# Performance work log

Hardware: AMD Instinct MI355X
Metric: run time of the kernel (lower is better)

Reference implementation:

```python
import jax, jax.numpy as jnp
import numpy as np

IN_DIM = 768
OUT_DIM = 4096
N_SK_ITER = 3
TARGET_TEMP = 0.06
PRED_TEMP = 0.12
PREFACTOR = 1.0
EXP_MAX = 50.0  # exp_max_values[float32]
SK_EPS = 1e-8
NORM_EPS = 1e-7


def setup_inputs() -> dict:
    key = jax.random.key(0)
    kx, kw = jax.random.split(key)
    x = jax.random.normal(kx, (16, 1024, IN_DIM), dtype=jnp.float32)
    # nn.Linear weight init: normal(std=1); bias zeros
    weight = jax.random.normal(kw, (OUT_DIM, IN_DIM), dtype=jnp.float32)
    bias = jnp.zeros((OUT_DIM,), dtype=jnp.float32)
    return {"x": x, "weight": weight, "bias": bias}


def sinkhorn_knopp(M, n_iterations, eps=SK_EPS):
    # stable_exp: shift by max over dim=-2 (token axis), add EXP_MAX
    shift = jnp.max(M, axis=-2, keepdims=True)
    M = jnp.exp(M + EXP_MAX - shift)
    for _ in range(n_iterations):  # small fixed count
        M = M / (jnp.sum(M, axis=-2, keepdims=True) + eps)  # column normalize
        M = M / (jnp.sum(M, axis=-1, keepdims=True) + eps)  # row normalize
    return M


def reference(x, weight, bias):
    # L2 normalize features (eps matches torch F.normalize with p=2)
    norm = jnp.maximum(jnp.linalg.norm(x, axis=-1, keepdims=True), NORM_EPS)
    x_n = x / norm
    logits = jnp.einsum("bnd,kd->bnk", x_n, weight) + bias  # [B, N, K]
    # positionwise_sk=True: no flatten before sinkhorn; detach -> stop_gradient
    assignments = sinkhorn_knopp(jax.lax.stop_gradient(logits) / TARGET_TEMP, N_SK_ITER)
    tgt = assignments.reshape(-1, OUT_DIM).astype(jnp.float32)
    pred = logits.reshape(-1, OUT_DIM).astype(jnp.float32)
    loss = -jnp.mean(jnp.sum(tgt * jax.nn.log_softmax(pred / PRED_TEMP, axis=-1), axis=-1))
    return assignments, PREFACTOR * loss
```

## Files before the change

kernel.cpp:

```cpp
#include <hip/hip_runtime.h>
#include <math.h>

#define BATCH 16
#define NTOK  1024
#define NCLU  4096
#define DIM   768
#define MROWS (BATCH * NTOK)

constexpr float TT_INV    = 16.666666666666668f;
constexpr float PT_INV    = 8.333333333333334f;
constexpr float SK_EPS_   = 1e-8f;
constexpr float NORM_EPS_ = 1e-7f;
constexpr float COL_SHIFT = 60.0f;
constexpr float P_SHIFT   = 40.0f;

typedef _Float16 f16x8 __attribute__((ext_vector_type(8)));
typedef _Float16 f16x4 __attribute__((ext_vector_type(4)));
typedef float    f32x4 __attribute__((ext_vector_type(4)));

struct F8 { float v[8]; };

__device__ __forceinline__ F8 load8(const float* p) {
    const float4 a = *(const float4*)p;
    const float4 b = *(const float4*)(p + 4);
    return F8{{a.x, a.y, a.z, a.w, b.x, b.y, b.z, b.w}};
}
__device__ __forceinline__ F8 load8(const _Float16* p) {
    f16x8 h = *(const f16x8*)p;
    F8 r;
#pragma unroll
    for (int i = 0; i < 8; ++i) r.v[i] = (float)h[i];
    return r;
}

__device__ __forceinline__ float wave_sum(float s) {
#pragma unroll
    for (int off = 32; off; off >>= 1) s += __shfl_xor(s, off);
    return s;
}

__device__ __forceinline__ void gl_lds16(const void* g, void* l) {
    __builtin_amdgcn_global_load_lds(
        (const __attribute__((address_space(1))) unsigned int*)g,
        (__attribute__((address_space(3))) unsigned int*)l,
        16, 0, 0);
}

__global__ __launch_bounds__(256) void castx_kernel(
    const float* __restrict__ x, _Float16* __restrict__ x16)
{
    int row  = (blockIdx.x * 256 + threadIdx.x) >> 6;
    int lane = threadIdx.x & 63;
    const float4* rp = (const float4*)(x + (size_t)row * DIM);
    float4 v[3];
    float ss = 0.f;
#pragma unroll
    for (int i = 0; i < 3; ++i) {
        v[i] = rp[lane + i * 64];
        ss += v[i].x * v[i].x + v[i].y * v[i].y + v[i].z * v[i].z + v[i].w * v[i].w;
    }
    ss = wave_sum(ss);
    float sc = 1.0f / fmaxf(sqrtf(ss), NORM_EPS_);
    _Float16* op = x16 + (size_t)row * DIM;
#pragma unroll
    for (int i = 0; i < 3; ++i) {
        f16x4 h;
        h[0] = (_Float16)(v[i].x * sc); h[1] = (_Float16)(v[i].y * sc);
        h[2] = (_Float16)(v[i].z * sc); h[3] = (_Float16)(v[i].w * sc);
        *(f16x4*)(op + 4 * (lane + i * 64)) = h;
    }
}

__global__ __launch_bounds__(256) void castw_kernel(
    const float* __restrict__ w, _Float16* __restrict__ w16)
{
    int i = blockIdx.x * 256 + threadIdx.x;
    const float4 a = *(const float4*)(w + (size_t)i * 8);
    const float4 b = *(const float4*)(w + (size_t)i * 8 + 4);
    f16x8 h;
    h[0] = (_Float16)a.x; h[1] = (_Float16)a.y; h[2] = (_Float16)a.z; h[3] = (_Float16)a.w;
    h[4] = (_Float16)b.x; h[5] = (_Float16)b.y; h[6] = (_Float16)b.z; h[7] = (_Float16)b.w;
    *(f16x8*)(w16 + (size_t)i * 8) = h;
}

__global__ __launch_bounds__(256) void rownorm_kernel(
    const float* __restrict__ x, float* __restrict__ invn)
{
    int wave = (blockIdx.x * 256 + threadIdx.x) >> 6;
    int lane = threadIdx.x & 63;
    const float4* row = (const float4*)(x + (size_t)wave * DIM);
    float s = 0.f;
#pragma unroll
    for (int i = 0; i < 3; ++i) {
        float4 v = row[lane + i * 64];
        s += v.x * v.x + v.y * v.y + v.z * v.z + v.w * v.w;
    }
    s = wave_sum(s);
    if (lane == 0) invn[wave] = 1.0f / fmaxf(sqrtf(s), NORM_EPS_);
}

#define BM 128
#define BN 128
#define BK 64
#define BKF 32

__global__ __launch_bounds__(256) void gemm16(
    const _Float16* __restrict__ A,
    const _Float16* __restrict__ B,
    const float* __restrict__ bias,
    _Float16* __restrict__ out,
    float* __restrict__ colpart)
{
    __shared__ __align__(16) _Float16 As[BM * BK];
    __shared__ __align__(16) _Float16 Bs[BN * BK];

    const int tid  = threadIdx.x;
    const int lane = tid & 63;
    const int wid  = tid >> 6;
    const int wr = wid >> 1, wc = wid & 1;

    const int nwg = gridDim.x;
    const int cpx = nwg >> 3;
    const int bid = blockIdx.x;
    const int swz = (bid & 7) * cpx + (bid >> 3);
    const int brow = (swz >> 5) * BM;
    const int bcol = (swz & 31) * BN;

    const int r8 = lane >> 3;
    const int s8 = lane & 7;
    const int srcslot = s8 ^ r8;

    const _Float16* gA = A + (size_t)(brow + wid * 32 + r8) * DIM + srcslot * 8;
    const _Float16* gB = B + (size_t)(bcol + wid * 32 + r8) * DIM + srcslot * 8;

    const int q  = lane >> 4;
    const int fr = lane & 15;
    const int fx = fr & 7;

    f32x4 acc[4][4] = {};

    const int NT = DIM / BK;
    for (int kt = 0; kt < NT; ++kt) {
        const size_t ko = (size_t)kt * BK;
        __syncthreads();
#pragma unroll
        for (int i = 0; i < 4; ++i) {
            gl_lds16(gA + (size_t)(i * 8) * DIM + ko, &As[(wid * 32 + i * 8) * BK]);
            gl_lds16(gB + (size_t)(i * 8) * DIM + ko, &Bs[(wid * 32 + i * 8) * BK]);
        }
        __syncthreads();

#pragma unroll
        for (int kk = 0; kk < 2; ++kk) {
            const int sA = ((kk * 4 + q) ^ fx) * 8;
            f16x8 af[4], bf[4];
#pragma unroll
            for (int m = 0; m < 4; ++m)
                af[m] = *(const f16x8*)&As[(wr * 64 + m * 16 + fr) * BK + sA];
#pragma unroll
            for (int n = 0; n < 4; ++n)
                bf[n] = *(const f16x8*)&Bs[(wc * 64 + n * 16 + fr) * BK + sA];
#pragma unroll
            for (int m = 0; m < 4; ++m)
#pragma unroll
                for (int n = 0; n < 4; ++n)
                    acc[m][n] = __builtin_amdgcn_mfma_f32_16x16x32_f16(
                        af[m], bf[n], acc[m][n], 0, 0, 0);
        }
    }

    float cs[4] = {0.f, 0.f, 0.f, 0.f};
#pragma unroll
    for (int n = 0; n < 4; ++n) {
        int col = bcol + wc * 64 + n * 16 + fr;
        float bv = bias[col];
#pragma unroll
        for (int m = 0; m < 4; ++m) {
            int row0 = brow + wr * 64 + m * 16 + (q << 2);
#pragma unroll
            for (int j = 0; j < 4; ++j) {
                float v = acc[m][n][j] + bv;
                out[(size_t)(row0 + j) * NCLU + col] = (_Float16)v;
                cs[n] += __expf(v * TT_INV - COL_SHIFT);
            }
        }
    }
    __syncthreads();
    float* cred = (float*)&As[0];
#pragma unroll
    for (int n = 0; n < 4; ++n) {
        float c2 = cs[n];
        c2 += __shfl_xor(c2, 16);
        c2 += __shfl_xor(c2, 32);
        if (q == 0) cred[((wr * 2 + wc) * 4 + n) * 16 + fr] = c2;
    }
    __syncthreads();
    if (tid < 128) {
        int wc2 = tid >> 6, n2 = (tid >> 4) & 3, fr2 = tid & 15;
        float S = cred[((0 * 2 + wc2) * 4 + n2) * 16 + fr2]
                + cred[((1 * 2 + wc2) * 4 + n2) * 16 + fr2];
        colpart[(size_t)(brow >> 7) * NCLU + bcol + wc2 * 64 + n2 * 16 + fr2] = S;
    }
}

__global__ __launch_bounds__(256) void colfin_kernel(
    const float* __restrict__ part, float* __restrict__ a1)
{
    int i = blockIdx.x * 256 + threadIdx.x;
    int b = i >> 12, k = i & (NCLU - 1);
    const float* p = part + (size_t)(b * 8) * NCLU + k;
    float s = 0.f;
#pragma unroll
    for (int rb = 0; rb < 8; ++rb) { s += *p; p += NCLU; }
    a1[i] = -COL_SHIFT - __logf(s);
}

template <bool FIRST>
__global__ __launch_bounds__(256) void rcpass_kernel(
    const _Float16* __restrict__ L, const float* __restrict__ a_in,
    const float* __restrict__ b_in, float* __restrict__ b_out,
    float* __restrict__ part)
{
    __shared__ float wgt_sh[16];
    const int tid  = threadIdx.x;
    const int lane = tid & 63;
    const int wv   = tid >> 6;
    const int chunk = blockIdx.x;
    const int b     = chunk >> 6;
    const int row0  = chunk * 16;
    const float* av = a_in + (size_t)b * NCLU;

    float ar[8][8];
#pragma unroll
    for (int i = 0; i < 8; ++i) {
        int c = i * 64 + lane;
        *(float4*)&ar[i][0] = *(const float4*)&av[c * 8];
        *(float4*)&ar[i][4] = *(const float4*)&av[c * 8 + 4];
    }

#pragma unroll
    for (int rr = 0; rr < 4; ++rr) {
        int row = row0 + wv * 4 + rr;
        const _Float16* Lr = L + (size_t)row * NCLU;
        float bp = FIRST ? 0.f : b_in[row];
        float s = 0.f;
#pragma unroll
        for (int i = 0; i < 8; ++i) {
            int c = i * 64 + lane;
            f16x8 h = *(const f16x8*)&Lr[c * 8];
#pragma unroll
            for (int j = 0; j < 8; ++j)
                s += __expf((float)h[j] * TT_INV + ar[i][j] + bp);
        }
        s = wave_sum(s);
        if (lane == 0) {
            float bn = bp - __logf(s + SK_EPS_);
            b_out[row] = bn;
            wgt_sh[wv * 4 + rr] = __expf(bn);
        }
    }
    __syncthreads();

    float aown[2][8];
#pragma unroll
    for (int sl = 0; sl < 2; ++sl) {
        *(float4*)&aown[sl][0] = *(const float4*)&av[sl * 2048 + tid * 8];
        *(float4*)&aown[sl][4] = *(const float4*)&av[sl * 2048 + tid * 8 + 4];
    }
    float acc[2][8] = {};
    for (int rr = 0; rr < 16; ++rr) {
        const _Float16* Lr = L + (size_t)(row0 + rr) * NCLU;
        float wg = wgt_sh[rr];
#pragma unroll
        for (int sl = 0; sl < 2; ++sl) {
            f16x8 h = *(const f16x8*)&Lr[sl * 2048 + tid * 8];
#pragma unroll
            for (int j = 0; j < 8; ++j)
                acc[sl][j] += __expf((float)h[j] * TT_INV + aown[sl][j]) * wg;
        }
    }
    float* P = part + (size_t)chunk * NCLU;
#pragma unroll
    for (int sl = 0; sl < 2; ++sl) {
        f32x4 w0, w1;
        w0[0] = acc[sl][0]; w0[1] = acc[sl][1]; w0[2] = acc[sl][2]; w0[3] = acc[sl][3];
        w1[0] = acc[sl][4]; w1[1] = acc[sl][5]; w1[2] = acc[sl][6]; w1[3] = acc[sl][7];
        *(f32x4*)&P[sl * 2048 + tid * 8]     = w0;
        *(f32x4*)&P[sl * 2048 + tid * 8 + 4] = w1;
    }
}

__global__ __launch_bounds__(256) void colfinN_kernel(
    const float* __restrict__ part, const float* __restrict__ a_in,
    float* __restrict__ a_out)
{
    int i = blockIdx.x * 256 + threadIdx.x;
    int b = i >> 12, k = i & (NCLU - 1);
    const float* p = part + (size_t)(b * 64) * NCLU + k;
    float s = 0.f;
#pragma unroll 8
    for (int c = 0; c < 64; ++c) { s += *p; p += NCLU; }
    a_out[i] = a_in[i] - __logf(s + SK_EPS_);
}

#define LDK 40

__device__ __forceinline__ f16x8 pack8(float4 lo, float4 hi, float sc) {
    f16x8 h;
    h[0] = (_Float16)(lo.x * sc); h[1] = (_Float16)(lo.y * sc);
    h[2] = (_Float16)(lo.z * sc); h[3] = (_Float16)(lo.w * sc);
    h[4] = (_Float16)(hi.x * sc); h[5] = (_Float16)(hi.y * sc);
    h[6] = (_Float16)(hi.z * sc); h[7] = (_Float16)(hi.w * sc);
    return h;
}

template <typename OT>
__global__ __launch_bounds__(256) void gemm_f16(
    const float* __restrict__ x, const float* __restrict__ w,
    const float* __restrict__ bias, const float* __restrict__ invn,
    OT* __restrict__ out)
{
    __shared__ __align__(16) _Float16 As[BM * LDK];
    __shared__ __align__(16) _Float16 Bs[BN * LDK];

    const int tid  = threadIdx.x;
    const int lane = tid & 63;
    const int wid  = tid >> 6;
    const int wr = wid >> 1, wc = wid & 1;
    const int brow = blockIdx.y * BM;
    const int bcol = blockIdx.x * BN;

    const int r0 = tid >> 2;
    const int r1 = r0 + 64;
    const int kc = (tid & 3) * 8;
    const float sA0 = invn[brow + r0];
    const float sA1 = invn[brow + r1];
    const float* gA0 = x + (size_t)(brow + r0) * DIM + kc;
    const float* gA1 = x + (size_t)(brow + r1) * DIM + kc;
    const float* gB0 = w + (size_t)(bcol + r0) * DIM + kc;
    const float* gB1 = w + (size_t)(bcol + r1) * DIM + kc;

    f32x4 acc[4][4] = {};
    float4 a00, a01, a10, a11, b00, b01, b10, b11;
    a00 = *(const float4*)(gA0);     a01 = *(const float4*)(gA0 + 4);
    a10 = *(const float4*)(gA1);     a11 = *(const float4*)(gA1 + 4);
    b00 = *(const float4*)(gB0);     b01 = *(const float4*)(gB0 + 4);
    b10 = *(const float4*)(gB1);     b11 = *(const float4*)(gB1 + 4);

    const int NT = DIM / BKF;
    for (int kt = 0; kt < NT; ++kt) {
        __syncthreads();
        *(f16x8*)&As[r0 * LDK + kc] = pack8(a00, a01, sA0);
        *(f16x8*)&As[r1 * LDK + kc] = pack8(a10, a11, sA1);
        *(f16x8*)&Bs[r0 * LDK + kc] = pack8(b00, b01, 1.0f);
        *(f16x8*)&Bs[r1 * LDK + kc] = pack8(b10, b11, 1.0f);
        __syncthreads();

        if (kt + 1 < NT) {
            int k0 = (kt + 1) * BKF;
            a00 = *(const float4*)(gA0 + k0); a01 = *(const float4*)(gA0 + k0 + 4);
            a10 = *(const float4*)(gA1 + k0); a11 = *(const float4*)(gA1 + k0 + 4);
            b00 = *(const float4*)(gB0 + k0); b01 = *(const float4*)(gB0 + k0 + 4);
            b10 = *(const float4*)(gB1 + k0); b11 = *(const float4*)(gB1 + k0 + 4);
        }

        const int ko = (lane >> 4) * 8;
        f16x8 af[4], bf[4];
#pragma unroll
        for (int m = 0; m < 4; ++m)
            af[m] = *(const f16x8*)&As[(wr * 64 + m * 16 + (lane & 15)) * LDK + ko];
#pragma unroll
        for (int n = 0; n < 4; ++n)
            bf[n] = *(const f16x8*)&Bs[(wc * 64 + n * 16 + (lane & 15)) * LDK + ko];
#pragma unroll
        for (int m = 0; m < 4; ++m)
#pragma unroll
            for (int n = 0; n < 4; ++n)
                acc[m][n] = __builtin_amdgcn_mfma_f32_16x16x32_f16(
                    af[m], bf[n], acc[m][n], 0, 0, 0);
    }

#pragma unroll
    for (int n = 0; n < 4; ++n) {
        int col = bcol + wc * 64 + n * 16 + (lane & 15);
        float bv = bias[col];
#pragma unroll
        for (int m = 0; m < 4; ++m) {
            int row0 = brow + wr * 64 + m * 16 + ((lane >> 4) << 2);
#pragma unroll
            for (int j = 0; j < 4; ++j)
                out[(size_t)(row0 + j) * NCLU + col] = (OT)(acc[m][n][j] + bv);
        }
    }
}

template <typename T>
__global__ __launch_bounds__(256) void colpass_kernel(
    const T* __restrict__ L, const float* __restrict__ a_in,
    const float* __restrict__ b_in, float* __restrict__ a_out)
{
    __shared__ float bsh[NTOK];
    __shared__ float ss[4][64];
    int b = blockIdx.x >> 6;
    int k = ((blockIdx.x & 63) << 6) + (threadIdx.x & 63);
    int wv = threadIdx.x >> 6;
    int lane = threadIdx.x & 63;
    const bool first = (b_in == nullptr);
    if (first) {
        for (int i = threadIdx.x; i < NTOK; i += 256) bsh[i] = 0.f;
    } else {
        for (int i = threadIdx.x; i < NTOK; i += 256) bsh[i] = b_in[b * NTOK + i];
    }
    __syncthreads();
    float aval = first ? -COL_SHIFT : a_in[b * NCLU + k];
    const T* p = L + (size_t)b * NTOK * NCLU + (size_t)(wv * 256) * NCLU + k;
    float s = 0.f;
#pragma unroll 4
    for (int n = 0; n < 256; ++n) {
        s += __expf((float)(*p) * TT_INV + aval + bsh[wv * 256 + n]);
        p += NCLU;
    }
    ss[wv][lane] = s;
    __syncthreads();
    if (wv == 0) {
        float S = ss[0][lane] + ss[1][lane] + ss[2][lane] + ss[3][lane];
        a_out[b * NCLU + k] = aval - __logf(first ? S : S + SK_EPS_);
    }
}

template <typename T>
__global__ __launch_bounds__(256) void colpassV_kernel(
    const T* __restrict__ L, const float* __restrict__ a_in,
    const float* __restrict__ b_in, float* __restrict__ a_out)
{
    __shared__ float bsh[NTOK];
    __shared__ float red[16][16][8];
    const int b     = blockIdx.x >> 5;
    const int strip = blockIdx.x & 31;
    const int cc    = threadIdx.x & 15;
    const int rg    = threadIdx.x >> 4;
    const int col0  = strip * 128 + cc * 8;
    for (int i = threadIdx.x; i < NTOK; i += 256) bsh[i] = b_in[b * NTOK + i];
    __syncthreads();
    const float4 av0 = *(const float4*)(a_in + b * NCLU + col0);
    const float4 av1 = *(const float4*)(a_in + b * NCLU + col0 + 4);
    const float av[8] = {av0.x, av0.y, av0.z, av0.w, av1.x, av1.y, av1.z, av1.w};
    float s[8] = {};
    const T* p = L + (size_t)b * NTOK * NCLU + (size_t)rg * NCLU + col0;
    for (int it = 0; it < 64; ++it) {
        F8 Lv = load8(p);
        float bpv = bsh[it * 16 + rg];
#pragma unroll
        for (int j = 0; j < 8; ++j) s[j] += __expf(Lv.v[j] * TT_INV + av[j] + bpv);
        p += (size_t)16 * NCLU;
    }
#pragma unroll
    for (int j = 0; j < 8; ++j) red[rg][cc][j] = s[j];
    __syncthreads();
    if (threadIdx.x < 128) {
        int c2 = threadIdx.x >> 3, j2 = threadIdx.x & 7;
        float S = 0.f;
#pragma unroll
        for (int g = 0; g < 16; ++g) S += red[g][c2][j2];
        int col = strip * 128 + c2 * 8 + j2;
        a_out[b * NCLU + col] = a_in[b * NCLU + col] - __logf(S + SK_EPS_);
    }
}

template <typename T>
__global__ __launch_bounds__(256) void rowpass_kernel(
    const T* __restrict__ L, const float* __restrict__ a_in,
    const float* __restrict__ b_in, float* __restrict__ b_out)
{
    int row  = (blockIdx.x * 256 + threadIdx.x) >> 6;
    int lane = threadIdx.x & 63;
    int b = row >> 10;
    const T* Lr = L + (size_t)row * NCLU;
    const float* av = a_in + (size_t)b * NCLU;
    float bp = b_in ? b_in[row] : 0.f;
    float s = 0.f;
#pragma unroll
    for (int i = 0; i < 8; ++i) {
        int c = i * 64 + lane;
        F8 Lv = load8(Lr + c * 8);
        F8 Av = load8(av + c * 8);
#pragma unroll
        for (int j = 0; j < 8; ++j)
            s += __expf(Lv.v[j] * TT_INV + Av.v[j] + bp);
    }
    s = wave_sum(s);
    if (lane == 0) b_out[row] = bp - __logf(s + SK_EPS_);
}

template <typename T>
__global__ __launch_bounds__(256) void final_kernel(
    const T* __restrict__ L, const float* __restrict__ a3,
    const float* __restrict__ b2, float* __restrict__ out,
    float* __restrict__ rowloss)
{
    __shared__ float red[3][4];
    const int row  = blockIdx.x;
    const int tid  = threadIdx.x;
    const int lane = tid & 63;
    const int wv   = tid >> 6;
    const int b    = row >> 10;
    const T* Lr = L + (size_t)row * NCLU;
    const float* av = a3 + (size_t)b * NCLU;
    const float bp = b2[row];

    float e[2][8];
    float rs = 0.f, q = 0.f, sP = 0.f;
#pragma unroll
    for (int jj = 0; jj < 2; ++jj) {
        int c = tid + jj * 256;
        F8 Lv = load8(Lr + c * 8);
        F8 Av = load8(av + c * 8);
#pragma unroll
        for (int j = 0; j < 8; ++j) {
            float P  = Lv.v[j] * PT_INV;
            float ev = __expf(Lv.v[j] * TT_INV + Av.v[j] + bp);
            e[jj][j] = ev;
            rs += ev;
            q  += ev * P;
            sP += __expf(P - P_SHIFT);
        }
    }
    rs = wave_sum(rs); q = wave_sum(q); sP = wave_sum(sP);
    if (lane == 0) { red[0][wv] = rs; red[1][wv] = q; red[2][wv] = sP; }
    __syncthreads();
    rs = red[0][0] + red[0][1] + red[0][2] + red[0][3];
    q  = red[1][0] + red[1][1] + red[1][2] + red[1][3];
    sP = red[2][0] + red[2][1] + red[2][2] + red[2][3];

    const float inv = 1.0f / (rs + SK_EPS_);
    const float lse = P_SHIFT + __logf(sP);

    float* Or = out + (size_t)row * NCLU;
#pragma unroll
    for (int jj = 0; jj < 2; ++jj) {
        int c = tid + jj * 256;
        f32x4 w0, w1;
        w0[0] = e[jj][0] * inv; w0[1] = e[jj][1] * inv;
        w0[2] = e[jj][2] * inv; w0[3] = e[jj][3] * inv;
        w1[0] = e[jj][4] * inv; w1[1] = e[jj][5] * inv;
        w1[2] = e[jj][6] * inv; w1[3] = e[jj][7] * inv;
        __builtin_nontemporal_store(w0, (f32x4*)(Or + c * 8));
        __builtin_nontemporal_store(w1, (f32x4*)(Or + c * 8 + 4));
    }
    if (tid == 0) rowloss[row] = q * inv - lse * (rs * inv);
}

__global__ __launch_bounds__(256) void lossred_kernel(
    const float* __restrict__ rowloss, float* __restrict__ out_loss)
{
    __shared__ float red[4];
    int tid = threadIdx.x, lane = tid & 63, wv = tid >> 6;
    float s = 0.f;
    for (int i = tid; i < MROWS; i += 256) s += rowloss[i];
    s = wave_sum(s);
    if (lane == 0) red[wv] = s;
    __syncthreads();
    if (tid == 0)
        out_loss[0] = -(red[0] + red[1] + red[2] + red[3]) / (float)MROWS;
}

extern "C" void kernel_launch(void* const* d_in, const int* in_sizes, int n_in,
                              void* d_out, int out_size, void* d_ws, size_t ws_size,
                              hipStream_t stream)
{
    const float* x    = (const float*)d_in[0];
    const float* w    = (const float*)d_in[1];
    const float* bias = (const float*)d_in[2];
    float* out = (float*)d_out;
    char* base = (char*)d_ws;
    float* ws  = (float*)d_ws;

    float* a1      = ws;
    float* a2      = a1 + BATCH * NCLU;
    float* a3      = a2 + BATCH * NCLU;
    float* b1      = a3 + BATCH * NCLU;
    float* b2      = b1 + MROWS;
    float* rowloss = b2 + MROWS;

    const size_t SMALL = 1u << 20;
    const size_t L16B  = (size_t)MROWS * NCLU * 2;
    const size_t X16B  = (size_t)MROWS * DIM * 2;
    const size_t W16B  = (size_t)NCLU * DIM * 2;
    const size_t PARTB = (size_t)128 * NCLU * 4;

    const int CB = BATCH * (NCLU / 64);
    const int RB = MROWS / 4;

    if (ws_size >= SMALL + L16B + X16B + W16B + PARTB) {
        _Float16* L16 = (_Float16*)(base + SMALL);
        _Float16* X16 = (_Float16*)(base + SMALL + L16B);
        _Float16* W16 = (_Float16*)(base + SMALL + L16B + X16B);
        float*    part1 = (float*)(base + SMALL + L16B + X16B + W16B);
        float*    part  = (float*)(base + SMALL + L16B);

        castx_kernel<<<MROWS / 4, 256, 0, stream>>>(x, X16);
        castw_kernel<<<(NCLU * DIM / 8) / 256, 256, 0, stream>>>(w, W16);
        gemm16<<<(MROWS / BM) * (NCLU / BN), 256, 0, stream>>>(X16, W16, bias, L16, part1);
        colfin_kernel<<<BATCH * NCLU / 256, 256, 0, stream>>>(part1, a1);
        rcpass_kernel<true ><<<MROWS / 16, 256, 0, stream>>>(L16, a1, nullptr, b1, part);
        colfinN_kernel<<<BATCH * NCLU / 256, 256, 0, stream>>>(part, a1, a2);
        rcpass_kernel<false><<<MROWS / 16, 256, 0, stream>>>(L16, a2, b1, b2, part);
        colfinN_kernel<<<BATCH * NCLU / 256, 256, 0, stream>>>(part, a2, a3);
        final_kernel<_Float16><<<MROWS, 256, 0, stream>>>(L16, a3, b2, out, rowloss);
        lossred_kernel<<<1, 256, 0, stream>>>(rowloss, out + (size_t)MROWS * NCLU);
    } else if (ws_size >= SMALL + L16B) {
        float* invn = rowloss + MROWS;
        _Float16* L16 = (_Float16*)(base + SMALL);
        rownorm_kernel<<<MROWS / 4, 256, 0, stream>>>(x, invn);
        dim3 gg(NCLU / BN, MROWS / BM);
        gemm_f16<_Float16><<<gg, 256, 0, stream>>>(x, w, bias, invn, L16);
        colpass_kernel<_Float16><<<CB, 256, 0, stream>>>(L16, nullptr, nullptr, a1);
        rowpass_kernel<_Float16><<<RB, 256, 0, stream>>>(L16, a1, nullptr, b1);
        colpassV_kernel<_Float16><<<BATCH * 32, 256, 0, stream>>>(L16, a1, b1, a2);
        rowpass_kernel<_Float16><<<RB, 256, 0, stream>>>(L16, a2, b1, b2);
        colpassV_kernel<_Float16><<<BATCH * 32, 256, 0, stream>>>(L16, a2, b2, a3);
        final_kernel<_Float16><<<MROWS, 256, 0, stream>>>(L16, a3, b2, out, rowloss);
        lossred_kernel<<<1, 256, 0, stream>>>(rowloss, out + (size_t)MROWS * NCLU);
    } else {
        float* invn = rowloss + MROWS;
        rownorm_kernel<<<MROWS / 4, 256, 0, stream>>>(x, invn);
        dim3 gg(NCLU / BN, MROWS / BM);
        gemm_f16<float><<<gg, 256, 0, stream>>>(x, w, bias, invn, out);
        colpass_kernel<float><<<CB, 256, 0, stream>>>(out, nullptr, nullptr, a1);
        rowpass_kernel<float><<<RB, 256, 0, stream>>>(out, a1, nullptr, b1);
        colpassV_kernel<float><<<BATCH * 32, 256, 0, stream>>>(out, a1, b1, a2);
        rowpass_kernel<float><<<RB, 256, 0, stream>>>(out, a2, b1, b2);
        colpassV_kernel<float><<<BATCH * 32, 256, 0, stream>>>(out, a2, b2, a3);
        final_kernel<float><<<MROWS, 256, 0, stream>>>(out, a3, b2, out, rowloss);
        lossred_kernel<<<1, 256, 0, stream>>>(rowloss, out + (size_t)MROWS * NCLU);
    }
}
```

Measured before the change: 356.6 us.

## Triple-buffer GEMM LDS tiles with BK=32 and async prefetch

The fp16 GEMM main loop moves from a single LDS buffer with two barriers per 64-wide k-step to a three-stage ring of 32-wide k tiles. The next tile's direct global-to-LDS loads are issued before computing the current one, with a manual vmcnt wait and one barrier per step. The LDS swizzle is redone for the narrower rows. This aims to hide global load latency behind MFMA work, at the cost of more barrier steps and fragile hand-written waitcnt ordering.

```diff
diff --git a/kernel.cpp b/kernel.cpp
--- a/kernel.cpp
+++ b/kernel.cpp
@@ -101,8 +101,9 @@
 
 #define BM 128
 #define BN 128
-#define BK 64
+#define BK 32
 #define BKF 32
+#define NT_ (DIM / BK)
 
 __global__ __launch_bounds__(256) void gemm16(
     const _Float16* __restrict__ A,
@@ -111,8 +112,8 @@
     _Float16* __restrict__ out,
     float* __restrict__ colpart)
 {
-    __shared__ __align__(16) _Float16 As[BM * BK];
-    __shared__ __align__(16) _Float16 Bs[BN * BK];
+    __shared__ __align__(16) _Float16 As[3][BM * BK];
+    __shared__ __align__(16) _Float16 Bs[3][BN * BK];
 
     const int tid  = threadIdx.x;
     const int lane = tid & 63;
@@ -126,48 +127,68 @@
     const int brow = (swz >> 5) * BM;
     const int bcol = (swz & 31) * BN;
 
-    const int r8 = lane >> 3;
-    const int s8 = lane & 7;
-    const int srcslot = s8 ^ r8;
-
-    const _Float16* gA = A + (size_t)(brow + wid * 32 + r8) * DIM + srcslot * 8;
-    const _Float16* gB = B + (size_t)(bcol + wid * 32 + r8) * DIM + srcslot * 8;
+    const int r2 = lane >> 2;
+    const int s2 = lane & 3;
+    const int srcslot = s2 ^ (r2 & 3) ^ ((lane >> 4) & 3);
+    const int sub0 = wid * 2, sub1 = wid * 2 + 1;
+
+    const _Float16* gA0 = A + (size_t)(brow + sub0 * 16 + r2) * DIM + srcslot * 8;
+    const _Float16* gA1 = A + (size_t)(brow + sub1 * 16 + r2) * DIM + srcslot * 8;
+    const _Float16* gB0 = B + (size_t)(bcol + sub0 * 16 + r2) * DIM + srcslot * 8;
+    const _Float16* gB1 = B + (size_t)(bcol + sub1 * 16 + r2) * DIM + srcslot * 8;
+    const int oA0 = sub0 * 16 * BK, oA1 = sub1 * 16 * BK;
 
     const int q  = lane >> 4;
     const int fr = lane & 15;
-    const int fx = fr & 7;
+    const int slot = q ^ (fr & 3) ^ ((fr >> 2) & 3);
+    const int aoff = (wr * 64 + fr) * BK + slot * 8;
+    const int boff = (wc * 64 + fr) * BK + slot * 8;
 
     f32x4 acc[4][4] = {};
 
-    const int NT = DIM / BK;
-    for (int kt = 0; kt < NT; ++kt) {
-        const size_t ko = (size_t)kt * BK;
-        __syncthreads();
-#pragma unroll
-        for (int i = 0; i < 4; ++i) {
-            gl_lds16(gA + (size_t)(i * 8) * DIM + ko, &As[(wid * 32 + i * 8) * BK]);
-            gl_lds16(gB + (size_t)(i * 8) * DIM + ko, &Bs[(wid * 32 + i * 8) * BK]);
-        }
-        __syncthreads();
-
-#pragma unroll
-        for (int kk = 0; kk < 2; ++kk) {
-            const int sA = ((kk * 4 + q) ^ fx) * 8;
-            f16x8 af[4], bf[4];
-#pragma unroll
-            for (int m = 0; m < 4; ++m)
-                af[m] = *(const f16x8*)&As[(wr * 64 + m * 16 + fr) * BK + sA];
-#pragma unroll
-            for (int n = 0; n < 4; ++n)
-                bf[n] = *(const f16x8*)&Bs[(wc * 64 + n * 16 + fr) * BK + sA];
-#pragma unroll
-            for (int m = 0; m < 4; ++m)
-#pragma unroll
-                for (int n = 0; n < 4; ++n)
-                    acc[m][n] = __builtin_amdgcn_mfma_f32_16x16x32_f16(
-                        af[m], bf[n], acc[m][n], 0, 0, 0);
-        }
-    }
+#define STAGE(bi, kn)                                   \
+    gl_lds16(gA0 + (kn), &As[bi][oA0]);                 \
+    gl_lds16(gA1 + (kn), &As[bi][oA1]);                 \
+    gl_lds16(gB0 + (kn), &Bs[bi][oA0]);                 \
+    gl_lds16(gB1 + (kn), &Bs[bi][oA1]);
+
+#define COMPUTE(bi)                                                        \
+    {                                                                      \
+        f16x8 af[4], bf[4];                                                \
+        _Pragma("unroll")                                                  \
+        for (int m = 0; m < 4; ++m)                                        \
+            af[m] = *(const f16x8*)&As[bi][aoff + m * 16 * BK];            \
+        _Pragma("unroll")                                                  \
+        for (int n = 0; n < 4; ++n)                                        \
+            bf[n] = *(const f16x8*)&Bs[bi][boff + n * 16 * BK];            \
+        _Pragma("unroll")                                                  \
+        for (int m = 0; m < 4; ++m)                                        \
+            _Pragma("unroll")                                              \
+            for (int n = 0; n < 4; ++n)                                    \
+                acc[m][n] = __builtin_amdgcn_mfma_f32_16x16x32_f16(        \
+                    af[m], bf[n], acc[m][n], 0, 0, 0);                     \
+    }
+
+#define BODY(t, bC, bS)                                                    \
+    {                                                                      \
+        const int kn = ((t) + 1 < NT_) ? ((t) + 1) * BK : 0;               \
+        STAGE(bS, kn);                                                     \
+        asm volatile("s_waitcnt vmcnt(4)" ::: "memory");                   \
+        __builtin_amdgcn_s_barrier();                                      \
+        asm volatile("" ::: "memory");                                     \
+        COMPUTE(bC);                                                       \
+    }
+
+    STAGE(0, 0);
+    for (int it = 0; it < NT_ / 3; ++it) {
+        const int t0 = it * 3;
+        BODY(t0,     0, 1);
+        BODY(t0 + 1, 1, 2);
+        BODY(t0 + 2, 2, 0);
+    }
+#undef BODY
+#undef COMPUTE
+#undef STAGE
 
     float cs[4] = {0.f, 0.f, 0.f, 0.f};
 #pragma unroll
@@ -186,7 +207,7 @@
         }
     }
     __syncthreads();
-    float* cred = (float*)&As[0];
+    float* cred = (float*)&As[0][0];
 #pragma unroll
     for (int n = 0; n < 4; ++n) {
         float c2 = cs[n];
```

Result: no change. 363.0 us (+1.8%).

## Rebuild fp16 GEMM with 256x256 tiles and a four-stage async LDS pipeline

Applied to the files above, without the earlier changes.

Replaces the 128x128, 256-thread GEMM with a 256x256-tile, 512-thread kernel. It uses a four-slot LDS ring filled by direct global-to-LDS loads and one barrier per K-step, gated by vmcnt waits, so loads overlap MFMA work. Each wave now holds a 128x64 accumulator block. The column-partial buffer and colfin reduction are resized for the new 256-row blocks. This should cut global traffic per FLOP and barrier stalls. The cost is higher register and LDS pressure (one workgroup per CU) and a few redundant wrap-around prefetch loads.

```diff
diff --git a/kernel.cpp b/kernel.cpp
--- a/kernel.cpp
+++ b/kernel.cpp
@@ -99,107 +99,128 @@
     if (lane == 0) invn[wave] = 1.0f / fmaxf(sqrtf(s), NORM_EPS_);
 }
 
-#define BM 128
-#define BN 128
-#define BK 64
-#define BKF 32
-
-__global__ __launch_bounds__(256) void gemm16(
+#define GKH   32
+#define NKH   (DIM / GKH)
+
+__global__ void __launch_bounds__(512, 1) gemm16(
     const _Float16* __restrict__ A,
     const _Float16* __restrict__ B,
     const float* __restrict__ bias,
     _Float16* __restrict__ out,
     float* __restrict__ colpart)
 {
-    __shared__ __align__(16) _Float16 As[BM * BK];
-    __shared__ __align__(16) _Float16 Bs[BN * BK];
+    __shared__ __align__(16) _Float16 AS[4][8192];
+    __shared__ __align__(16) _Float16 BS[4][8192];
 
     const int tid  = threadIdx.x;
     const int lane = tid & 63;
     const int wid  = tid >> 6;
-    const int wr = wid >> 1, wc = wid & 1;
+    const int wm   = wid >> 2;
+    const int wn   = wid & 3;
 
     const int nwg = gridDim.x;
     const int cpx = nwg >> 3;
-    const int bid = blockIdx.x;
-    const int swz = (bid & 7) * cpx + (bid >> 3);
-    const int brow = (swz >> 5) * BM;
-    const int bcol = (swz & 31) * BN;
-
-    const int r8 = lane >> 3;
-    const int s8 = lane & 7;
-    const int srcslot = s8 ^ r8;
-
-    const _Float16* gA = A + (size_t)(brow + wid * 32 + r8) * DIM + srcslot * 8;
-    const _Float16* gB = B + (size_t)(bcol + wid * 32 + r8) * DIM + srcslot * 8;
+    const int swz = (blockIdx.x & 7) * cpx + (blockIdx.x >> 3);
+    const int brow = (swz >> 4) * 256;
+    const int bcol = (swz & 15) * 256;
+
+    const int G0 = tid, G1 = tid + 512;
+    const int pr0 = G0 >> 3, s0 = G0 & 7;
+    const int rr0 = pr0 * 2 + (s0 >> 2), qq0 = (s0 & 3) ^ (pr0 & 3);
+    const int pr1 = G1 >> 3, s1 = G1 & 7;
+    const int rr1 = pr1 * 2 + (s1 >> 2), qq1 = (s1 & 3) ^ (pr1 & 3);
+
+    const _Float16* sA0 = A + (size_t)(brow + rr0) * DIM + qq0 * 8;
+    const _Float16* sA1 = A + (size_t)(brow + rr1) * DIM + qq1 * 8;
+    const _Float16* sB0 = B + (size_t)(bcol + rr0) * DIM + qq0 * 8;
+    const _Float16* sB1 = B + (size_t)(bcol + rr1) * DIM + qq1 * 8;
+    const int ldsOff0 = wid * 512;
+    const int ldsOff1 = wid * 512 + 4096;
 
     const int q  = lane >> 4;
     const int fr = lane & 15;
-    const int fx = fr & 7;
-
-    f32x4 acc[4][4] = {};
-
-    const int NT = DIM / BK;
-    for (int kt = 0; kt < NT; ++kt) {
-        const size_t ko = (size_t)kt * BK;
-        __syncthreads();
-#pragma unroll
-        for (int i = 0; i < 4; ++i) {
-            gl_lds16(gA + (size_t)(i * 8) * DIM + ko, &As[(wid * 32 + i * 8) * BK]);
-            gl_lds16(gB + (size_t)(i * 8) * DIM + ko, &Bs[(wid * 32 + i * 8) * BK]);
-        }
-        __syncthreads();
-
-#pragma unroll
-        for (int kk = 0; kk < 2; ++kk) {
-            const int sA = ((kk * 4 + q) ^ fx) * 8;
-            f16x8 af[4], bf[4];
-#pragma unroll
-            for (int m = 0; m < 4; ++m)
-                af[m] = *(const f16x8*)&As[(wr * 64 + m * 16 + fr) * BK + sA];
-#pragma unroll
-            for (int n = 0; n < 4; ++n)
-                bf[n] = *(const f16x8*)&Bs[(wc * 64 + n * 16 + fr) * BK + sA];
-#pragma unroll
-            for (int m = 0; m < 4; ++m)
-#pragma unroll
-                for (int n = 0; n < 4; ++n)
-                    acc[m][n] = __builtin_amdgcn_mfma_f32_16x16x32_f16(
-                        af[m], bf[n], acc[m][n], 0, 0, 0);
-        }
-    }
-
-    float cs[4] = {0.f, 0.f, 0.f, 0.f};
+    const int qp = q ^ ((fr >> 1) & 3);
+    const int fbase = ((fr & 1) * 4 + qp) * 8;
+    const int abase = (wm * 64 + (fr >> 1)) * 64 + fbase;
+    const int bbase = (wn * 32 + (fr >> 1)) * 64 + fbase;
+
+    f32x4 acc[8][4] = {};
+
+#define STAGE4(slot, kh) {                                  \
+    const int ko_ = (kh) * GKH;                             \
+    gl_lds16(sA0 + ko_, &AS[slot][ldsOff0]);                \
+    gl_lds16(sA1 + ko_, &AS[slot][ldsOff1]);                \
+    gl_lds16(sB0 + ko_, &BS[slot][ldsOff0]);                \
+    gl_lds16(sB1 + ko_, &BS[slot][ldsOff1]); }
+
+#define PHASE(slotC, slotS, khS) {                                         \
+    STAGE4(slotS, khS);                                                    \
+    asm volatile("s_waitcnt vmcnt(8)" ::: "memory");                       \
+    __builtin_amdgcn_s_barrier();                                          \
+    asm volatile("" ::: "memory");                                         \
+    f16x8 af[8], bf[4];                                                    \
+    _Pragma("unroll")                                                      \
+    for (int m = 0; m < 8; ++m)                                            \
+        af[m] = *(const f16x8*)&AS[slotC][abase + m * 512];                \
+    _Pragma("unroll")                                                      \
+    for (int n = 0; n < 4; ++n)                                            \
+        bf[n] = *(const f16x8*)&BS[slotC][bbase + n * 512];                \
+    _Pragma("unroll")                                                      \
+    for (int m = 0; m < 8; ++m)                                            \
+        _Pragma("unroll")                                                  \
+        for (int n = 0; n < 4; ++n)                                        \
+            acc[m][n] = __builtin_amdgcn_mfma_f32_16x16x32_f16(            \
+                af[m], bf[n], acc[m][n], 0, 0, 0); }
+
+    STAGE4(0, 0);
+    STAGE4(1, 1);
+
+    for (int i6 = 0; i6 < 6; ++i6) {
+        const int i = i6 * 4;
+        const int kh2 = i + 2;
+        const int kh3 = i + 3;
+        const int kh4 = (i + 4 < NKH) ? i + 4 : i + 4 - NKH;
+        const int kh5 = (i + 5 < NKH) ? i + 5 : i + 5 - NKH;
+        PHASE(0, 2, kh2);
+        PHASE(1, 3, kh3);
+        PHASE(2, 0, kh4);
+        PHASE(3, 1, kh5);
+    }
+#undef PHASE
+#undef STAGE4
+
+    __syncthreads();
+
+    float cred_local[4];
 #pragma unroll
     for (int n = 0; n < 4; ++n) {
-        int col = bcol + wc * 64 + n * 16 + fr;
+        int col = bcol + wn * 64 + n * 16 + fr;
         float bv = bias[col];
-#pragma unroll
-        for (int m = 0; m < 4; ++m) {
-            int row0 = brow + wr * 64 + m * 16 + (q << 2);
+        float cs = 0.f;
+#pragma unroll
+        for (int m = 0; m < 8; ++m) {
+            int row0 = brow + wm * 128 + m * 16 + (q << 2);
 #pragma unroll
             for (int j = 0; j < 4; ++j) {
                 float v = acc[m][n][j] + bv;
                 out[(size_t)(row0 + j) * NCLU + col] = (_Float16)v;
-                cs[n] += __expf(v * TT_INV - COL_SHIFT);
+                cs += __expf(v * TT_INV - COL_SHIFT);
             }
         }
-    }
-    __syncthreads();
-    float* cred = (float*)&As[0];
-#pragma unroll
-    for (int n = 0; n < 4; ++n) {
-        float c2 = cs[n];
-        c2 += __shfl_xor(c2, 16);
-        c2 += __shfl_xor(c2, 32);
-        if (q == 0) cred[((wr * 2 + wc) * 4 + n) * 16 + fr] = c2;
-    }
-    __syncthreads();
-    if (tid < 128) {
-        int wc2 = tid >> 6, n2 = (tid >> 4) & 3, fr2 = tid & 15;
-        float S = cred[((0 * 2 + wc2) * 4 + n2) * 16 + fr2]
-                + cred[((1 * 2 + wc2) * 4 + n2) * 16 + fr2];
-        colpart[(size_t)(brow >> 7) * NCLU + bcol + wc2 * 64 + n2 * 16 + fr2] = S;
+        cs += __shfl_xor(cs, 16);
+        cs += __shfl_xor(cs, 32);
+        cred_local[n] = cs;
+    }
+    float* cred = (float*)&AS[0][0];
+#pragma unroll
+    for (int n = 0; n < 4; ++n)
+        if (q == 0) cred[((wm * 4 + wn) * 4 + n) * 16 + fr] = cred_local[n];
+    __syncthreads();
+    if (tid < 256) {
+        int wn2 = tid >> 6, n2 = (tid >> 4) & 3, fr2 = tid & 15;
+        float S = cred[((0 * 4 + wn2) * 4 + n2) * 16 + fr2]
+                + cred[((1 * 4 + wn2) * 4 + n2) * 16 + fr2];
+        colpart[(size_t)(swz >> 4) * NCLU + bcol + wn2 * 64 + n2 * 16 + fr2] = S;
     }
 }
 
@@ -208,10 +229,10 @@
 {
     int i = blockIdx.x * 256 + threadIdx.x;
     int b = i >> 12, k = i & (NCLU - 1);
-    const float* p = part + (size_t)(b * 8) * NCLU + k;
+    const float* p = part + (size_t)(b * 4) * NCLU + k;
     float s = 0.f;
 #pragma unroll
-    for (int rb = 0; rb < 8; ++rb) { s += *p; p += NCLU; }
+    for (int rb = 0; rb < 4; ++rb) { s += *p; p += NCLU; }
     a1[i] = -COL_SHIFT - __logf(s);
 }
 
@@ -303,6 +324,9 @@
     a_out[i] = a_in[i] - __logf(s + SK_EPS_);
 }
 
+#define BM 128
+#define BN 128
+#define BKF 32
 #define LDK 40
 
 __device__ __forceinline__ f16x8 pack8(float4 lo, float4 hi, float sc) {
@@ -586,7 +610,7 @@
     const size_t L16B  = (size_t)MROWS * NCLU * 2;
     const size_t X16B  = (size_t)MROWS * DIM * 2;
     const size_t W16B  = (size_t)NCLU * DIM * 2;
-    const size_t PARTB = (size_t)128 * NCLU * 4;
+    const size_t PARTB = (size_t)64 * NCLU * 4;
 
     const int CB = BATCH * (NCLU / 64);
     const int RB = MROWS / 4;
@@ -600,7 +624,7 @@
 
         castx_kernel<<<MROWS / 4, 256, 0, stream>>>(x, X16);
         castw_kernel<<<(NCLU * DIM / 8) / 256, 256, 0, stream>>>(w, W16);
-        gemm16<<<(MROWS / BM) * (NCLU / BN), 256, 0, stream>>>(X16, W16, bias, L16, part1);
+        gemm16<<<(MROWS / 256) * (NCLU / 256), 512, 0, stream>>>(X16, W16, bias, L16, part1);
         colfin_kernel<<<BATCH * NCLU / 256, 256, 0, stream>>>(part1, a1);
         rcpass_kernel<true ><<<MROWS / 16, 256, 0, stream>>>(L16, a1, nullptr, b1, part);
         colfinN_kernel<<<BATCH * NCLU / 256, 256, 0, stream>>>(part, a1, a2);
```

Result: faster. 341.0 us (-4.4%).
